# Performance work log

Hardware: AMD Instinct MI355X
Metric: run time of the kernel (lower is better)

## Reference

```python
import jax, jax.numpy as jnp
import numpy as np

N = 8192      # number of samples (x.shape[0])
D = 64        # out_feat / spectral embedding dim
K_NN = 32     # config['school']['k']
KP1 = 64      # columns in idx (>= K_NN + 1)
N_PROJ_ITERS = 100  # Newton iterations for simplex projection


def setup_inputs() -> dict:
    key = jax.random.key(0)
    k1, k2, k3, k4 = jax.random.split(key, 4)
    Y = jax.random.normal(k1, (N, D), jnp.float32)
    semantic_H = jax.random.normal(k2, (N, D), jnp.float32)
    ortho_H = jax.random.normal(k3, (N, D), jnp.float32)
    idx = jax.random.randint(k4, (N, KP1), 0, N)
    return {"Y": Y, "semantic_H": semantic_H, "ortho_H": ortho_H,
            "idx": idx, "alpha": 1, "beta": 1}


def eproj_simplex_rows(v, k=1.0):
    """Project each row of v onto the simplex {x >= 0, sum(x) = k}.
    Fixed-iteration Newton solve for the Lagrange multiplier (matches the
    iterative EProjSimplex_new_matrix; it is a fixed point once converged)."""
    n = v.shape[1]
    v0 = v - v.mean(axis=1, keepdims=True) + k / n   # shift so sum(v0) = k per row

    def body(_, lam):
        v1 = v0 - lam[:, None]
        pos = v1 > 0
        npos = jnp.maximum(pos.sum(axis=1), 1)       # -g
        f = jnp.where(pos, v1, 0.0).sum(axis=1) - k  # constraint residual
        return lam + f / npos                         # lam - f/g

    lam = jax.lax.fori_loop(0, N_PROJ_ITERS, body,
                            jnp.zeros(v.shape[0], v.dtype))
    return jnp.maximum(v0 - lam[:, None], 0.0)


def reference(Y, semantic_H, ortho_H, idx, alpha, beta):
    num = Y.shape[0]
    idxa0 = idx[:, 1:K_NN + 1]                                   # [N, k]
    # kNN gather + pairwise L2 distances (O(N*k*d), no dense NxN distances)
    dfi = jnp.sqrt(((Y[:, None, :] - Y[idxa0]) ** 2).sum(-1) + 1e-8)          # [N, k]
    dxi = jnp.sqrt(((ortho_H[:, None, :] - ortho_H[idxa0]) ** 2).sum(-1) + 1e-8)
    ad = -(dxi + beta * dfi) / (2 * alpha)
    w = eproj_simplex_rows(ad)                                   # [N, k] simplex weights
    # scatter into dense NxN adjacency (faithful to A.scatter_(1, idxa0, w))
    rows = jnp.arange(num)[:, None]
    A = jnp.zeros((num, num), Y.dtype).at[rows, idxa0].set(w)
    embs_hom = A @ semantic_H                                    # [N, D]
    return embs_hom, A, Y
```

## Files before the change

### kernel.cpp

```cpp
#include <hip/hip_runtime.h>

#define NROWS 8192
#define DDIM  64
#define KNN   32
#define MAXIT 100

__device__ __forceinline__ float scalar_val(const void* p) {
    int iv = *(const int*)p;
    if (iv > -1000000 && iv < 1000000) return (float)iv;
    return *(const float*)p;
}

__global__ __launch_bounds__(256, 4) void school_fused_kernel(
    const float* __restrict__ Y,
    const float* __restrict__ semH,
    const float* __restrict__ orthoH,
    const int*   __restrict__ idx,
    const void*  alpha_p,
    const void*  beta_p,
    float* __restrict__ embs,
    float* __restrict__ A,
    float* __restrict__ Yout)
{
    __shared__ int    col_s[8][KNN];
    __shared__ float  ad_s[8][KNN];
    __shared__ float2 cw_s[8][KNN];

    const int tid  = threadIdx.x;
    const int j    = tid & 31;
    const int r    = tid >> 5;
    const int row0 = blockIdx.x * 8;
    const int row  = row0 + r;

    const float alpha = scalar_val(alpha_p);
    const float beta  = scalar_val(beta_p);

    const int col = idx[row * 64 + 1 + j];
    col_s[r][j] = col;

    const float4* Y4 = (const float4*)Y;
    const float4* O4 = (const float4*)orthoH;
    const int p = j & 3;
    const int Q = j >> 2;

    float4 oy0 = Y4[(size_t)row * 16 + p +  0];
    float4 oy1 = Y4[(size_t)row * 16 + p +  4];
    float4 oy2 = Y4[(size_t)row * 16 + p +  8];
    float4 oy3 = Y4[(size_t)row * 16 + p + 12];
    float4 oo0 = O4[(size_t)row * 16 + p +  0];
    float4 oo1 = O4[(size_t)row * 16 + p +  4];
    float4 oo2 = O4[(size_t)row * 16 + p +  8];
    float4 oo3 = O4[(size_t)row * 16 + p + 12];

    #pragma unroll 2
    for (int b = 0; b < 4; ++b) {
        const int cidx = b * 8 + Q;
        const int c = col_s[r][cidx];
        float dY = 0.f, dO = 0.f;
        #define ACC_PH(ph, oy, oo)                                          \
        {                                                                   \
            float4 gY = Y4[(size_t)c * 16 + p + 4 * ph];                    \
            float4 gO = O4[(size_t)c * 16 + p + 4 * ph];                    \
            float ex = oy.x - gY.x, ey = oy.y - gY.y,                       \
                  ez = oy.z - gY.z, ew = oy.w - gY.w;                       \
            dY += ex * ex + ey * ey + ez * ez + ew * ew;                    \
            ex = oo.x - gO.x; ey = oo.y - gO.y;                             \
            ez = oo.z - gO.z; ew = oo.w - gO.w;                             \
            dO += ex * ex + ey * ey + ez * ez + ew * ew;                    \
        }
        ACC_PH(0, oy0, oo0)
        ACC_PH(1, oy1, oo1)
        ACC_PH(2, oy2, oo2)
        ACC_PH(3, oy3, oo3)
        #undef ACC_PH
        dY += __shfl_xor(dY, 1, 64);
        dY += __shfl_xor(dY, 2, 64);
        dO += __shfl_xor(dO, 1, 64);
        dO += __shfl_xor(dO, 2, 64);
        if (p == 0) {
            float dfv = sqrtf(dY + 1e-8f);
            float dxv = sqrtf(dO + 1e-8f);
            ad_s[r][cidx] = -(dxv + beta * dfv) / (2.f * alpha);
        }
    }
    const float ad = ad_s[r][j];

    float s = ad;
    #pragma unroll
    for (int mm = 1; mm <= 16; mm <<= 1) s += __shfl_xor(s, mm, 64);
    const float v0 = ad - s * (1.f / 32.f) + (1.f / 32.f);

    const unsigned long long halfmask = 0xFFFFFFFFull << (tid & 32);
    float lam = 0.f;
    #pragma unroll 1
    for (int it = 0; it < MAXIT; ++it) {
        float v1 = v0 - lam;
        bool pos = v1 > 0.f;
        float pp = pos ? v1 : 0.f;
        #pragma unroll
        for (int mm = 1; mm <= 16; mm <<= 1) pp += __shfl_xor(pp, mm, 64);
        float c = (float)__popcll(__ballot(pos ? 1 : 0) & halfmask);
        float step = (pp - 1.f) / fmaxf(c, 1.f);
        lam += step;
        if (__all(fabsf(step) <= 1e-6f ? 1 : 0)) break;
    }
    const float w = fmaxf(v0 - lam, 0.f);

    bool dead = false;
    for (int jj = j + 1; jj < 32; ++jj)
        dead |= (col_s[r][jj] == col);
    cw_s[r][j] = make_float2(__int_as_float(col), dead ? 0.f : w);

    {
        float2 acc = make_float2(0.f, 0.f);
        const float2* H2 = (const float2*)semH;
        #pragma unroll 4
        for (int jj = 0; jj < KNN; ++jj) {
            float2 cw = cw_s[r][jj];
            int   c   = __float_as_int(cw.x);
            float wv  = cw.y;
            float2 h = H2[(size_t)c * 32 + j];
            acc.x += wv * h.x;
            acc.y += wv * h.y;
        }
        ((float2*)embs)[(size_t)row * 32 + j] = acc;
    }

    {
        const float2* Y2 = (const float2*)(Y + (size_t)row0 * DDIM);
        float2* O2 = (float2*)(Yout + (size_t)row0 * DDIM);
        O2[tid] = Y2[tid];
    }

    unsigned k0 = 0xFFFFFFFFu, k1 = 0xFFFFFFFFu, k2 = 0xFFFFFFFFu, k3 = 0xFFFFFFFFu;
    float f0 = 0.f, f1 = 0.f, f2 = 0.f, f3 = 0.f;
    int nhit = 0;
    #pragma unroll 1
    for (int jj = 0; jj < 32; ++jj) {
        float2 cw = cw_s[r][jj];
        int c = __float_as_int(cw.x);
        if (((c >> 2) & 31) == j) {
            unsigned key = ((unsigned)(c >> 7) << 2) | (unsigned)(c & 3);
            float wv = cw.y;
            k3 = (nhit == 3) ? key : k3;  f3 = (nhit == 3) ? wv : f3;
            k2 = (nhit == 2) ? key : k2;  f2 = (nhit == 2) ? wv : f2;
            k1 = (nhit == 1) ? key : k1;  f1 = (nhit == 1) ? wv : f1;
            k0 = (nhit == 0) ? key : k0;  f0 = (nhit == 0) ? wv : f0;
            nhit++;
        }
    }

    {
        float4* Arow4 = (float4*)(A + (size_t)row * NROWS);
        #pragma unroll 4
        for (int ss = 0; ss < 64; ++ss) {
            float4 v = make_float4(0.f, 0.f, 0.f, 0.f);
            #define APPLY_SLOT(kk, ff)                                   \
                if ((kk >> 2) == (unsigned)ss) {                         \
                    int p_ = (int)(kk & 3u);                             \
                    v.x = (p_ == 0) ? ff : v.x;                          \
                    v.y = (p_ == 1) ? ff : v.y;                          \
                    v.z = (p_ == 2) ? ff : v.z;                          \
                    v.w = (p_ == 3) ? ff : v.w;                          \
                }
            APPLY_SLOT(k0, f0)
            APPLY_SLOT(k1, f1)
            APPLY_SLOT(k2, f2)
            APPLY_SLOT(k3, f3)
            #undef APPLY_SLOT
            Arow4[(ss << 5) + j] = v;
        }
    }

    if (nhit > 4) {
        asm volatile("s_waitcnt vmcnt(0)" ::: "memory");
        int cnt = 0;
        for (int jj = 0; jj < 32; ++jj) {
            float2 cw = cw_s[r][jj];
            int c = __float_as_int(cw.x);
            if (((c >> 2) & 31) == j) {
                if (cnt >= 4) {
                    A[(size_t)row * NROWS + c] = cw.y;
                    asm volatile("s_waitcnt vmcnt(0)" ::: "memory");
                }
                cnt++;
            }
        }
    }
}

extern "C" void kernel_launch(void* const* d_in, const int* in_sizes, int n_in,
                              void* d_out, int out_size, void* d_ws, size_t ws_size,
                              hipStream_t stream) {
    const float* Y      = (const float*)d_in[0];
    const float* semH   = (const float*)d_in[1];
    const float* orthoH = (const float*)d_in[2];
    const int*   idx    = (const int*)d_in[3];
    const void*  alpha  = d_in[4];
    const void*  beta   = d_in[5];

    float* out  = (float*)d_out;
    float* embs = out;
    float* A    = out + (size_t)NROWS * DDIM;
    float* Yout = A + (size_t)NROWS * NROWS;

    school_fused_kernel<<<NROWS / 8, 256, 0, stream>>>(
        Y, semH, orthoH, idx, alpha, beta, embs, A, Yout);
}
```

Baseline: 60.16 us.

## Issue zero-fill of A and semH gathers before simplex projection loop

Computes a per-lane hitmask of which A row chunks hold neighbor columns, then writes zeros to all other chunks before the Newton projection loop, so the bulk of the store traffic overlaps with the iterative compute. The semantic_H gathers are prefetched into a 32-entry register array ahead of the loop, and the Y copy is moved earlier. After the weights are known, only the chunks flagged in the hitmask are written with weights. This raises register pressure, which may lower occupancy, and it adds sched_barriers.

Result: slower. 65.73 us (+9.3%).

```diff
diff --git a/kernel.cpp b/kernel.cpp
--- a/kernel.cpp
+++ b/kernel.cpp
@@ -37,6 +37,13 @@
 
     const int col = idx[row * 64 + 1 + j];
     col_s[r][j] = col;
+
+    unsigned long long hitmask = 0ull;
+    #pragma unroll 1
+    for (int jj = 0; jj < 32; ++jj) {
+        int c = col_s[r][jj];
+        if (((c >> 2) & 31) == j) hitmask |= 1ull << (c >> 7);
+    }
 
     const float4* Y4 = (const float4*)Y;
     const float4* O4 = (const float4*)orthoH;
@@ -85,6 +92,36 @@
     }
     const float ad = ad_s[r][j];
 
+    {
+        const float2* Y2 = (const float2*)(Y + (size_t)row0 * DDIM);
+        float2* O2 = (float2*)(Yout + (size_t)row0 * DDIM);
+        O2[tid] = Y2[tid];
+    }
+
+    float2 h_arr[32];
+    {
+        const float2* H2 = (const float2*)semH;
+        #pragma unroll
+        for (int jj = 0; jj < KNN; ++jj) {
+            int c = col_s[r][jj];
+            h_arr[jj] = H2[(size_t)c * 32 + j];
+        }
+    }
+
+    __builtin_amdgcn_sched_barrier(0);
+
+    {
+        const float4 z4 = make_float4(0.f, 0.f, 0.f, 0.f);
+        float4* Arow4 = (float4*)(A + (size_t)row * NROWS);
+        #pragma unroll 8
+        for (int ss = 0; ss < 64; ++ss) {
+            if (!((hitmask >> ss) & 1ull))
+                Arow4[(ss << 5) + j] = z4;
+        }
+    }
+
+    __builtin_amdgcn_sched_barrier(0);
+
     float s = ad;
     #pragma unroll
     for (int mm = 1; mm <= 16; mm <<= 1) s += __shfl_xor(s, mm, 64);
@@ -110,27 +147,6 @@
     for (int jj = j + 1; jj < 32; ++jj)
         dead |= (col_s[r][jj] == col);
     cw_s[r][j] = make_float2(__int_as_float(col), dead ? 0.f : w);
-
-    {
-        float2 acc = make_float2(0.f, 0.f);
-        const float2* H2 = (const float2*)semH;
-        #pragma unroll 4
-        for (int jj = 0; jj < KNN; ++jj) {
-            float2 cw = cw_s[r][jj];
-            int   c   = __float_as_int(cw.x);
-            float wv  = cw.y;
-            float2 h = H2[(size_t)c * 32 + j];
-            acc.x += wv * h.x;
-            acc.y += wv * h.y;
-        }
-        ((float2*)embs)[(size_t)row * 32 + j] = acc;
-    }
-
-    {
-        const float2* Y2 = (const float2*)(Y + (size_t)row0 * DDIM);
-        float2* O2 = (float2*)(Yout + (size_t)row0 * DDIM);
-        O2[tid] = Y2[tid];
-    }
 
     unsigned k0 = 0xFFFFFFFFu, k1 = 0xFFFFFFFFu, k2 = 0xFFFFFFFFu, k3 = 0xFFFFFFFFu;
     float f0 = 0.f, f1 = 0.f, f2 = 0.f, f3 = 0.f;
@@ -151,12 +167,25 @@
     }
 
     {
+        float2 acc = make_float2(0.f, 0.f);
+        #pragma unroll
+        for (int jj = 0; jj < KNN; ++jj) {
+            float wv = cw_s[r][jj].y;
+            acc.x += wv * h_arr[jj].x;
+            acc.y += wv * h_arr[jj].y;
+        }
+        ((float2*)embs)[(size_t)row * 32 + j] = acc;
+    }
+
+    {
         float4* Arow4 = (float4*)(A + (size_t)row * NROWS);
-        #pragma unroll 4
-        for (int ss = 0; ss < 64; ++ss) {
+        unsigned long long mrem = hitmask;
+        while (mrem) {
+            int ss = __ffsll(mrem) - 1;
+            mrem &= mrem - 1;
             float4 v = make_float4(0.f, 0.f, 0.f, 0.f);
             #define APPLY_SLOT(kk, ff)                                   \
-                if ((kk >> 2) == (unsigned)ss) {                         \
+                if ((int)(kk >> 2) == ss) {                              \
                     int p_ = (int)(kk & 3u);                             \
                     v.x = (p_ == 0) ? ff : v.x;                          \
                     v.y = (p_ == 1) ? ff : v.y;                          \
```
